# Kernel tuning notes

Measured on AMD Instinct MI355X. Metric: run time of the kernel, lower is better.

Reference implementation:

```python
import jax, jax.numpy as jnp
import numpy as np

D_MODEL = 1024
NUM_HEADS = 16
HEAD_DIM = D_MODEL // NUM_HEADS
B, S = 2, 2048
EPS = 1e-8


def setup_inputs() -> dict:
    key = jax.random.key(0)
    ks = jax.random.split(key, 9)
    sc = 1.0 / np.sqrt(D_MODEL)
    return {
        "x": jax.random.normal(ks[0], (B, S, D_MODEL), jnp.float32),
        "wq": jax.random.normal(ks[1], (D_MODEL, D_MODEL), jnp.float32) * sc,
        "bq": jax.random.normal(ks[2], (D_MODEL,), jnp.float32) * 0.01,
        "wk": jax.random.normal(ks[3], (D_MODEL, D_MODEL), jnp.float32) * sc,
        "bk": jax.random.normal(ks[4], (D_MODEL,), jnp.float32) * 0.01,
        "wv": jax.random.normal(ks[5], (D_MODEL, D_MODEL), jnp.float32) * sc,
        "bv": jax.random.normal(ks[6], (D_MODEL,), jnp.float32) * 0.01,
        "wo": jax.random.normal(ks[7], (D_MODEL, D_MODEL), jnp.float32) * sc,
        "bo": jax.random.normal(ks[8], (D_MODEL,), jnp.float32) * 0.01,
    }


def reference(x, wq, bq, wk, bk, wv, bv, wo, bo):
    b, s, d = x.shape
    h, hd = NUM_HEADS, HEAD_DIM
    # projections (torch Linear: y = x W^T + b); reshape to [b, h, s, hd]
    def proj(w, bias):
        return (jnp.einsum('bsd,ed->bse', x, w) + bias).reshape(b, s, h, hd).transpose(0, 2, 1, 3)
    q = proj(wq, bq)
    k = proj(wk, bk)
    v = proj(wv, bv)
    scores = jnp.einsum('bhqd,bhkd->bhqk', q, k) / np.sqrt(hd)
    attn = jax.nn.softmax(scores, axis=-1)
    o = jnp.einsum('bhqk,bhkd->bhqd', attn, v)  # [b, h, s, hd]
    # per-position, per-head Gram-Schmidt exclusion: remove component of o[i]
    # along v[i] (the loop in the original is independent over positions)
    v_norm_sq = jnp.sum(v * v, axis=-1, keepdims=True)          # [b,h,s,1]
    align = jnp.sum(o * v, axis=-1, keepdims=True) / (v_norm_sq + EPS)
    o = o - align * v
    o = o.transpose(0, 2, 1, 3).reshape(b, s, d)
    return jnp.einsum('bsd,ed->bse', o, wo) + bo
```

## Files before the change

kernel.cpp:

```cpp
#include <hip/hip_runtime.h>
#include <stdint.h>

#define SEQ 2048
#define NTOK 4096
#define DM 1024

typedef __bf16 bf16x8 __attribute__((ext_vector_type(8)));
typedef __bf16 bf16x4 __attribute__((ext_vector_type(4)));
typedef float f32x4 __attribute__((ext_vector_type(4)));

__device__ __forceinline__ unsigned short f2bf(float f) {
  union { float f; unsigned u; } v; v.f = f;
  return (unsigned short)((v.u + 0x7fffu + ((v.u >> 16) & 1u)) >> 16);
}
__device__ __forceinline__ float bf2f(unsigned short s) {
  union { unsigned u; float f; } v; v.u = ((unsigned)s) << 16; return v.f;
}
__device__ __forceinline__ unsigned pkbf(float a, float b) {
  union { float f; unsigned u; } x, y; x.f = a; y.f = b;
  return __builtin_amdgcn_perm(y.u + 0x8000u, x.u + 0x8000u, 0x07060302u);
}

__device__ __forceinline__ void async16(const unsigned short* g, unsigned short* l) {
  __builtin_amdgcn_global_load_lds(
      (const __attribute__((address_space(1))) void*)g,
      (__attribute__((address_space(3))) void*)l, 16, 0, 0);
}

__global__ __launch_bounds__(256) void cast_all(
    const float* __restrict__ x, const float* __restrict__ wq,
    const float* __restrict__ wk, const float* __restrict__ wv,
    const float* __restrict__ wo, unsigned short* __restrict__ dst) {
  size_t i = ((size_t)blockIdx.x * 256 + threadIdx.x) * 4;
  const float* src; size_t off;
  if (i < (size_t)NTOK * DM) { src = x; off = i; }
  else {
    size_t j = i - (size_t)NTOK * DM;
    int s = (int)(j >> 20);
    src = (s == 0) ? wq : (s == 1) ? wk : (s == 2) ? wv : wo;
    off = j & 1048575u;
  }
  float4 f = *(const float4*)(src + off);
  ushort4 o;
  o.x = f2bf(f.x); o.y = f2bf(f.y); o.z = f2bf(f.z); o.w = f2bf(f.w);
  *(ushort4*)(dst + i) = o;
}


template<int MI>
__device__ __forceinline__ void stage_half(
    const unsigned short* __restrict__ A, const unsigned short* __restrict__ Bw,
    int m0, int n0, int kt, unsigned short* As, unsigned short* Bs) {
  const int tid = threadIdx.x;
  const int r = tid >> 2, c = tid & 3;
#pragma unroll
  for (int b = 0; b < MI / 2; ++b) {
    const int row = b * 64 + r;
    async16(A + (size_t)(m0 + row) * 1024 + kt + ((c ^ (row & 3)) << 3),
            As + row * 32 + c * 8);
  }
#pragma unroll
  for (int b = 0; b < 2; ++b) {
    const int row = b * 64 + r;
    async16(Bw + (size_t)(n0 + row) * 1024 + kt + ((c ^ (row & 3)) << 3),
            Bs + row * 32 + c * 8);
  }
}

__device__ __forceinline__ void pipe_bar0() {
  asm volatile("s_waitcnt vmcnt(0)\ns_barrier" ::: "memory");
}
template<int MI>
__device__ __forceinline__ void pipe_barN() {
  if constexpr (MI == 4) asm volatile("s_waitcnt vmcnt(4)\ns_barrier" ::: "memory");
  else                   asm volatile("s_waitcnt vmcnt(3)\ns_barrier" ::: "memory");
}

template<int MI>
__device__ __forceinline__ void gemm_pipe(
    const unsigned short* __restrict__ A, const unsigned short* __restrict__ Bw,
    int m0, int n0, f32x4 (&acc)[MI][4],
    unsigned short* AsBase, unsigned short* BsBase) {
  const int tid = threadIdx.x, lane = tid & 63, w = tid >> 6;
  const int wm16 = (w >> 1) * MI * 16, wn = (w & 1) * 64;
  const int quad = lane >> 4, l16 = lane & 15;
  constexpr int ASZ = MI * 32 * 32;
  constexpr int BSZ = 128 * 32;

  stage_half<MI>(A, Bw, m0, n0, 0,  AsBase,       BsBase);
  stage_half<MI>(A, Bw, m0, n0, 32, AsBase + ASZ, BsBase + BSZ);
  pipe_barN<MI>();

  int cur = 0;
  for (int p = 0; p < 32; ++p) {
    const unsigned short* As = AsBase + cur * ASZ;
    const unsigned short* Bs = BsBase + cur * BSZ;

    bf16x8 af[MI], bf[4];
    const int swz = ((quad ^ (l16 & 3)) << 3);
#pragma unroll
    for (int i = 0; i < MI; ++i)
      af[i] = *(const bf16x8*)(As + (wm16 + i * 16 + l16) * 32 + swz);
#pragma unroll
    for (int j = 0; j < 4; ++j)
      bf[j] = *(const bf16x8*)(Bs + (wn + j * 16 + l16) * 32 + swz);

    if (p + 2 < 32) {
      const int slot = (cur == 0) ? 2 : cur - 1;
      stage_half<MI>(A, Bw, m0, n0, (p + 2) * 32,
                     AsBase + slot * ASZ, BsBase + slot * BSZ);
    }

#pragma unroll
    for (int i = 0; i < MI; ++i)
#pragma unroll
      for (int j = 0; j < 4; ++j)
        acc[i][j] = __builtin_amdgcn_mfma_f32_16x16x32_bf16(af[i], bf[j], acc[i][j], 0, 0, 0);

    if (p < 30)       pipe_barN<MI>();
    else if (p == 30) pipe_bar0();
    cur = (cur == 2) ? 0 : cur + 1;
  }
}

__device__ __forceinline__ void stage_half_qk(
    const unsigned short* __restrict__ A, const unsigned short* __restrict__ Bq,
    const unsigned short* __restrict__ Bk,
    int m0, int n0, int kt, unsigned short* As, unsigned short* Bqs,
    unsigned short* Bks) {
  const int tid = threadIdx.x;
  const int r = tid >> 2, c = tid & 3;
#pragma unroll
  for (int b = 0; b < 2; ++b) {
    const int row = b * 64 + r;
    const int off = kt + ((c ^ (row & 3)) << 3);
    async16(A + (size_t)(m0 + row) * 1024 + off, As + row * 32 + c * 8);
    async16(Bq + (size_t)(n0 + row) * 1024 + off, Bqs + row * 32 + c * 8);
    async16(Bk + (size_t)(n0 + row) * 1024 + off, Bks + row * 32 + c * 8);
  }
}
__device__ __forceinline__ void pipe_barQK() {
  asm volatile("s_waitcnt vmcnt(6)\ns_barrier" ::: "memory");
}

__device__ __forceinline__ void gemm_pipe_qk(
    const unsigned short* __restrict__ A, const unsigned short* __restrict__ Bq,
    const unsigned short* __restrict__ Bk,
    int m0, int n0, f32x4 (&accQ)[4][4], f32x4 (&accK)[4][4],
    unsigned short* AsBase, unsigned short* BqBase, unsigned short* BkBase) {
  const int tid = threadIdx.x, lane = tid & 63, w = tid >> 6;
  const int wm16 = (w >> 1) * 64, wn = (w & 1) * 64;
  const int quad = lane >> 4, l16 = lane & 15;
  constexpr int SZ = 128 * 32;

  stage_half_qk(A, Bq, Bk, m0, n0, 0,  AsBase,      BqBase,      BkBase);
  stage_half_qk(A, Bq, Bk, m0, n0, 32, AsBase + SZ, BqBase + SZ, BkBase + SZ);
  pipe_barQK();

  int cur = 0;
  for (int p = 0; p < 32; ++p) {
    const unsigned short* As = AsBase + cur * SZ;
    const unsigned short* Bqs = BqBase + cur * SZ;
    const unsigned short* Bks = BkBase + cur * SZ;

    bf16x8 af[4], bq[4], bk[4];
    const int swz = ((quad ^ (l16 & 3)) << 3);
#pragma unroll
    for (int i = 0; i < 4; ++i)
      af[i] = *(const bf16x8*)(As + (wm16 + i * 16 + l16) * 32 + swz);
#pragma unroll
    for (int j = 0; j < 4; ++j) {
      bq[j] = *(const bf16x8*)(Bqs + (wn + j * 16 + l16) * 32 + swz);
      bk[j] = *(const bf16x8*)(Bks + (wn + j * 16 + l16) * 32 + swz);
    }

    if (p + 2 < 32) {
      const int slot = (cur == 0) ? 2 : cur - 1;
      stage_half_qk(A, Bq, Bk, m0, n0, (p + 2) * 32,
                    AsBase + slot * SZ, BqBase + slot * SZ, BkBase + slot * SZ);
    }

#pragma unroll
    for (int i = 0; i < 4; ++i)
#pragma unroll
      for (int j = 0; j < 4; ++j) {
        accQ[i][j] = __builtin_amdgcn_mfma_f32_16x16x32_bf16(af[i], bq[j], accQ[i][j], 0, 0, 0);
        accK[i][j] = __builtin_amdgcn_mfma_f32_16x16x32_bf16(af[i], bk[j], accK[i][j], 0, 0, 0);
      }

    if (p < 30)       pipe_barQK();
    else if (p == 30) pipe_bar0();
    cur = (cur == 2) ? 0 : cur + 1;
  }
}

__global__ __launch_bounds__(256, 2) void qkv_gemm(
    const unsigned short* __restrict__ xb,
    const unsigned short* __restrict__ wqb, const unsigned short* __restrict__ wkb,
    const unsigned short* __restrict__ wvb,
    const float* __restrict__ bq, const float* __restrict__ bk, const float* __restrict__ bv,
    unsigned short* __restrict__ Q, unsigned short* __restrict__ Kd,
    unsigned short* __restrict__ Vt) {
  __shared__ unsigned short SH[9 * 128 * 32];
  const int gx = blockIdx.x;
  const int rr = gx & 255;
  const int tok = 4 * (rr & 7) + ((rr >> 3) & 3);
  const int oth = rr >> 5;
  const int lane = threadIdx.x & 63, w = threadIdx.x >> 6;
  const int quad = lane >> 4, l16 = lane & 15;
  const int wm = (w >> 1) * 64, wn = (w & 1) * 64;

  if (gx < 256) {
    const int m0 = tok * 128, n0 = oth * 128;
    f32x4 accQ[4][4], accK[4][4];
#pragma unroll
    for (int i = 0; i < 4; ++i)
#pragma unroll
      for (int j = 0; j < 4; ++j) {
        f32x4 z = {0.f, 0.f, 0.f, 0.f};
        accQ[i][j] = z; accK[i][j] = z;
      }
    gemm_pipe_qk(xb, wqb, wkb, m0, n0, accQ, accK,
                 SH, SH + 3 * 4096, SH + 6 * 4096);

#pragma unroll
    for (int i = 0; i < 4; ++i)
#pragma unroll
      for (int j = 0; j < 4; ++j) {
        const int col = n0 + wn + j * 16 + l16;
        const float bbq = bq[col], bbk = bk[col];
        const int h = col >> 6, d = col & 63;
#pragma unroll
        for (int r = 0; r < 4; ++r) {
          const int m = m0 + wm + i * 16 + quad * 4 + r;
          const int b = m >> 11, s = m & 2047;
          const int bh = b * 16 + h;
          Q[((size_t)bh * SEQ + s) * 64 + d] =
              f2bf((accQ[i][j][r] + bbq) * 0.180336880f);
          Kd[((size_t)bh * SEQ + s) * 64 + d] = f2bf(accK[i][j][r] + bbk);
        }
      }
  } else {
    const int m0 = oth * 128, n0 = tok * 128;
    f32x4 acc[4][4];
#pragma unroll
    for (int i = 0; i < 4; ++i)
#pragma unroll
      for (int j = 0; j < 4; ++j) { f32x4 z = {0.f, 0.f, 0.f, 0.f}; acc[i][j] = z; }
    gemm_pipe<4>(wvb, xb, m0, n0, acc, SH, SH + 3 * 4096);

#pragma unroll
    for (int i = 0; i < 4; ++i)
#pragma unroll
      for (int j = 0; j < 4; ++j) {
        const int n = n0 + wn + j * 16 + l16;
        const int tb = n >> 11, s = n & 2047;
#pragma unroll
        for (int r = 0; r < 4; ++r) {
          const int m = m0 + wm + i * 16 + quad * 4 + r;
          const int h = m >> 6, d = m & 63;
          Vt[((size_t)(tb * 16 + h) * 64 + d) * SEQ + s] = f2bf(acc[i][j][r] + bv[m]);
        }
      }
  }
}

__global__ __launch_bounds__(256, 2) void attn_kernel(
    const unsigned short* __restrict__ Q, const unsigned short* __restrict__ Kd,
    const unsigned short* __restrict__ Vt,
    unsigned short* __restrict__ O) {
  __shared__ unsigned short SH[32768];
#define KKB(g, b) (SH + ((g) * 2 + (b)) * 4096)
#define VVB(g, b) (SH + 16384 + ((g) * 2 + (b)) * 4096)
  const int gx = blockIdx.x;
  const int xcd = gx & 7;
  const int idx = gx >> 3;
  const int bh  = xcd * 4 + (idx & 3);
  const int q0  = (idx >> 2) * 128;
  const int tid = threadIdx.x, lane = tid & 63, w = tid >> 6;
  const int kp = w >> 1;
  const int wq = w & 1;
  const int quad = lane >> 4, l16 = lane & 15;
  const unsigned short* Qp = Q + (size_t)bh * SEQ * 64;
  const unsigned short* Kp = Kd + (size_t)bh * SEQ * 64;
  const unsigned short* Vp = Vt + (size_t)bh * 64 * SEQ;
  const int srow = tid >> 3;
  const int sc = ((tid & 7) ^ ((srow & 3) | ((srow & 8) >> 1))) << 3;

#pragma unroll
  for (int c = 0; c < 4; ++c)
    async16(Qp + (size_t)(q0 + c * 32 + srow) * 64 + sc,
            KKB(0, c >> 1) + (c & 1) * 2048 + tid * 8);
  __syncthreads();

  const int gl = (l16 & 3) | ((l16 & 8) >> 1);
  const int sel = l16 & 7;
  const unsigned short* Qsrc = KKB(0, wq);
  bf16x8 bQ[4][2];
#pragma unroll
  for (int qq = 0; qq < 4; ++qq) {
    const int qrow = qq * 16 + l16;
#pragma unroll
    for (int hh = 0; hh < 2; ++hh)
      bQ[qq][hh] = *(const bf16x8*)(Qsrc + qrow * 64 + (((hh * 4 + quad) ^ gl) << 3));
  }
  __syncthreads();

  auto stageKV = [&](int it_, int nb) {
#pragma unroll
    for (int g = 0; g < 2; ++g) {
      const int kt = g * 1024 + it_ * 64;
      async16(Kp + (size_t)(kt + srow) * 64 + sc, KKB(g, nb) + tid * 8);
      async16(Kp + (size_t)(kt + 32 + srow) * 64 + sc, KKB(g, nb) + 2048 + tid * 8);
      async16(Vp + (size_t)srow * SEQ + kt + sc, VVB(g, nb) + tid * 8);
      async16(Vp + (size_t)(32 + srow) * SEQ + kt + sc, VVB(g, nb) + 2048 + tid * 8);
    }
  };
  stageKV(0, 0);

  union { unsigned short u[8]; bf16x8 v; } one8;
#pragma unroll
  for (int t = 0; t < 8; ++t) one8.u[t] = 0x3F80;
  const bf16x8 aOnes = one8.v;

  f32x4 o_acc[4][4];
  f32x4 l_acc[4];
  const f32x4 zinit = {-12.f, -12.f, -12.f, -12.f};
#pragma unroll
  for (int qq = 0; qq < 4; ++qq) {
    f32x4 z = {0.f, 0.f, 0.f, 0.f};
    l_acc[qq] = z;
#pragma unroll
    for (int dt = 0; dt < 4; ++dt) o_acc[qq][dt] = z;
  }

  for (int it = 0; it < 16; ++it) {
    const int cur = it & 1;
    __syncthreads();
    if (it + 1 < 16) stageKV(it + 1, (it + 1) & 1);
    const unsigned short* Ks = KKB(kp, cur);
    const unsigned short* Vs = VVB(kp, cur);

    __builtin_amdgcn_s_setprio(1);

    bf16x8 bP[4][2];
#pragma unroll
    for (int ee = 0; ee < 4; ++ee) {
      const int G = ee >> 1, e = ee & 1;
      const int R = G * 32 + ((l16 >> 2) << 3) + e * 4 + (l16 & 3);
      const unsigned short* arow = Ks + R * 64;
      bf16x8 a0 = *(const bf16x8*)(arow + ((quad ^ sel) << 3));
      bf16x8 a1 = *(const bf16x8*)(arow + (((4 + quad) ^ sel) << 3));
#pragma unroll
      for (int qq = 0; qq < 4; ++qq) {
        f32x4 z = __builtin_amdgcn_mfma_f32_16x16x32_bf16(a0, bQ[qq][0], zinit, 0, 0, 0);
        z = __builtin_amdgcn_mfma_f32_16x16x32_bf16(a1, bQ[qq][1], z, 0, 0, 0);
        const unsigned u0 = (unsigned)(int)__builtin_fmaf(z[0], 8388608.0f, 1065024977.0f);
        const unsigned u1 = (unsigned)(int)__builtin_fmaf(z[1], 8388608.0f, 1065024977.0f);
        const unsigned u2 = (unsigned)(int)__builtin_fmaf(z[2], 8388608.0f, 1065024977.0f);
        const unsigned u3 = (unsigned)(int)__builtin_fmaf(z[3], 8388608.0f, 1065024977.0f);
        union { unsigned d[4]; bf16x8 v; } pk;
        pk.v = bP[qq][G];
        pk.d[e * 2]     = __builtin_amdgcn_perm(u1, u0, 0x07060302u);
        pk.d[e * 2 + 1] = __builtin_amdgcn_perm(u3, u2, 0x07060302u);
        bP[qq][G] = pk.v;
      }
    }

#pragma unroll
    for (int qq = 0; qq < 4; ++qq)
#pragma unroll
      for (int G = 0; G < 2; ++G)
        l_acc[qq] = __builtin_amdgcn_mfma_f32_16x16x32_bf16(aOnes, bP[qq][G], l_acc[qq], 0, 0, 0);

#pragma unroll
    for (int dt = 0; dt < 4; ++dt) {
      const unsigned short* vbase = Vs + (dt * 16 + l16) * 64;
#pragma unroll
      for (int G = 0; G < 2; ++G) {
        bf16x8 aV = *(const bf16x8*)(vbase + (((G * 4 + quad) ^ gl) << 3));
#pragma unroll
        for (int qq = 0; qq < 4; ++qq)
          o_acc[qq][dt] = __builtin_amdgcn_mfma_f32_16x16x32_bf16(aV, bP[qq][G], o_acc[qq][dt], 0, 0, 0);
      }
    }

    __builtin_amdgcn_s_setprio(0);
  }

  __syncthreads();
  float* xf = (float*)SH;
  if (kp == 1) {
    float* dst = xf + (size_t)(wq * 64 + lane) * 68;
#pragma unroll
    for (int qq = 0; qq < 4; ++qq)
#pragma unroll
      for (int dt = 0; dt < 4; ++dt)
        *(f32x4*)(dst + qq * 16 + dt * 4) = o_acc[qq][dt];
    f32x4 lv = {l_acc[0][0], l_acc[1][0], l_acc[2][0], l_acc[3][0]};
    *(f32x4*)(dst + 64) = lv;
  }
  __syncthreads();
  if (kp == 0) {
    const float* src = xf + (size_t)(wq * 64 + lane) * 68;
#pragma unroll
    for (int qq = 0; qq < 4; ++qq)
#pragma unroll
      for (int dt = 0; dt < 4; ++dt)
        o_acc[qq][dt] += *(const f32x4*)(src + qq * 16 + dt * 4);
    const f32x4 lv = *(const f32x4*)(src + 64);

    const int b = bh >> 4, h = bh & 15;
#pragma unroll
    for (int qq = 0; qq < 4; ++qq) {
      const int qg = q0 + wq * 64 + qq * 16 + l16;
      const float inv = 1.0f / (l_acc[qq][0] + lv[qq]);
      const unsigned short* vp = Vp + qg;
      float ov = 0.f, v2 = 0.f;
#pragma unroll
      for (int dt = 0; dt < 4; ++dt)
#pragma unroll
        for (int r = 0; r < 4; ++r) {
          const int d = dt * 16 + quad * 4 + r;
          const float v = bf2f(vp[(size_t)d * SEQ]);
          ov += o_acc[qq][dt][r] * v;
          v2 += v * v;
        }
      ov *= inv;
      ov += __shfl_xor(ov, 16); ov += __shfl_xor(ov, 32);
      v2 += __shfl_xor(v2, 16); v2 += __shfl_xor(v2, 32);
      const float align = ov / (v2 + 1e-8f);
      unsigned short* dst = O + (size_t)(b * SEQ + qg) * DM + h * 64;
#pragma unroll
      for (int dt = 0; dt < 4; ++dt) {
        float a[4];
#pragma unroll
        for (int r = 0; r < 4; ++r) {
          const int d = dt * 16 + quad * 4 + r;
          const float v = bf2f(vp[(size_t)d * SEQ]);
          a[r] = __builtin_fmaf(o_acc[qq][dt][r], inv, -align * v);
        }
        uint2 pk2;
        pk2.x = pkbf(a[0], a[1]);
        pk2.y = pkbf(a[2], a[3]);
        *(uint2*)(dst + dt * 16 + quad * 4) = pk2;
      }
    }
  }
#undef KKB
#undef VVB
}

__global__ __launch_bounds__(256) void out_gemm(
    const unsigned short* __restrict__ Ob, const unsigned short* __restrict__ wob,
    const float* __restrict__ bo, float* __restrict__ out) {
  __shared__ unsigned short As[3 * 64 * 32], Bs[3 * 128 * 32];
  const int m0 = blockIdx.y * 64, n0 = blockIdx.x * 128;
  f32x4 acc[2][4];
#pragma unroll
  for (int i = 0; i < 2; ++i)
#pragma unroll
    for (int j = 0; j < 4; ++j) { f32x4 z = {0.f, 0.f, 0.f, 0.f}; acc[i][j] = z; }

  gemm_pipe<2>(Ob, wob, m0, n0, acc, As, Bs);

  const int lane = threadIdx.x & 63, w = threadIdx.x >> 6;
  const int quad = lane >> 4, l16 = lane & 15;
  const int wm = (w >> 1) * 32, wn = (w & 1) * 64;
#pragma unroll
  for (int i = 0; i < 2; ++i)
#pragma unroll
    for (int j = 0; j < 4; ++j) {
      const int col = n0 + wn + j * 16 + l16;
      const float bb = bo[col];
#pragma unroll
      for (int r = 0; r < 4; ++r) {
        const int m = m0 + wm + i * 16 + quad * 4 + r;
        out[(size_t)m * DM + col] = acc[i][j][r] + bb;
      }
    }
}

extern "C" void kernel_launch(void* const* d_in, const int* in_sizes, int n_in,
                              void* d_out, int out_size, void* d_ws, size_t ws_size,
                              hipStream_t stream) {
  const float* x  = (const float*)d_in[0];
  const float* wq = (const float*)d_in[1];
  const float* bq = (const float*)d_in[2];
  const float* wk = (const float*)d_in[3];
  const float* bk = (const float*)d_in[4];
  const float* wv = (const float*)d_in[5];
  const float* bv = (const float*)d_in[6];
  const float* wo = (const float*)d_in[7];
  const float* bo = (const float*)d_in[8];
  float* out = (float*)d_out;
  (void)in_sizes; (void)n_in; (void)out_size; (void)ws_size;

  unsigned short* ws  = (unsigned short*)d_ws;
  unsigned short* xb  = ws;
  unsigned short* wqb = xb + (size_t)NTOK * DM;
  unsigned short* wkb = wqb + (size_t)DM * DM;
  unsigned short* wvb = wkb + (size_t)DM * DM;
  unsigned short* wob = wvb + (size_t)DM * DM;
  unsigned short* Qb  = wob + (size_t)DM * DM;
  unsigned short* Kb  = Qb + (size_t)NTOK * DM;
  unsigned short* Vtb = Kb + (size_t)NTOK * DM;
  unsigned short* Ob  = Vtb + (size_t)NTOK * DM;

  cast_all<<<8192, 256, 0, stream>>>(x, wq, wk, wv, wo, ws);
  qkv_gemm<<<512, 256, 0, stream>>>(xb, wqb, wkb, wvb, bq, bk, bv, Qb, Kb, Vtb);
  attn_kernel<<<512, 256, 0, stream>>>(Qb, Kb, Vtb, Ob);
  out_gemm<<<dim3(8, 64), 256, 0, stream>>>(Ob, wob, bo, out);
}
```

Before: 177.7 us.

## Software-pipeline attention loop: overlap PV MFMAs of previous tile with QK of current

Restructures the KV loop so the P·V and row-sum MFMAs for iteration it-1 run after the QK score computation of iteration it. V fragments and the packed P values are carried in registers across iterations, with an epilogue after the loop. The goal is to overlap the exp/pack ALU work with independent matrix instructions and hide LDS latency for V. The cost is more live registers (extra bf16x8 arrays plus an unroll of 2), which could lower occupancy or cause spills.

```diff
diff --git a/kernel.cpp b/kernel.cpp
--- a/kernel.cpp
+++ b/kernel.cpp
@@ -334,6 +334,10 @@
     for (int dt = 0; dt < 4; ++dt) o_acc[qq][dt] = z;
   }
 
+  bf16x8 bPo[4][2];
+  bf16x8 aVo[4][2];
+
+#pragma unroll 2
   for (int it = 0; it < 16; ++it) {
     const int cur = it & 1;
     __syncthreads();
@@ -343,7 +347,7 @@
 
     __builtin_amdgcn_s_setprio(1);
 
-    bf16x8 bP[4][2];
+    bf16x8 bPn[4][2];
 #pragma unroll
     for (int ee = 0; ee < 4; ++ee) {
       const int G = ee >> 1, e = ee & 1;
@@ -360,33 +364,58 @@
         const unsigned u2 = (unsigned)(int)__builtin_fmaf(z[2], 8388608.0f, 1065024977.0f);
         const unsigned u3 = (unsigned)(int)__builtin_fmaf(z[3], 8388608.0f, 1065024977.0f);
         union { unsigned d[4]; bf16x8 v; } pk;
-        pk.v = bP[qq][G];
+        pk.v = bPn[qq][G];
         pk.d[e * 2]     = __builtin_amdgcn_perm(u1, u0, 0x07060302u);
         pk.d[e * 2 + 1] = __builtin_amdgcn_perm(u3, u2, 0x07060302u);
-        bP[qq][G] = pk.v;
-      }
-    }
-
-#pragma unroll
-    for (int qq = 0; qq < 4; ++qq)
-#pragma unroll
-      for (int G = 0; G < 2; ++G)
-        l_acc[qq] = __builtin_amdgcn_mfma_f32_16x16x32_bf16(aOnes, bP[qq][G], l_acc[qq], 0, 0, 0);
+        bPn[qq][G] = pk.v;
+      }
+    }
+
+    if (it > 0) {
+#pragma unroll
+      for (int qq = 0; qq < 4; ++qq)
+#pragma unroll
+        for (int G = 0; G < 2; ++G)
+          l_acc[qq] = __builtin_amdgcn_mfma_f32_16x16x32_bf16(aOnes, bPo[qq][G], l_acc[qq], 0, 0, 0);
+#pragma unroll
+      for (int dt = 0; dt < 4; ++dt)
+#pragma unroll
+        for (int G = 0; G < 2; ++G)
+#pragma unroll
+          for (int qq = 0; qq < 4; ++qq)
+            o_acc[qq][dt] = __builtin_amdgcn_mfma_f32_16x16x32_bf16(aVo[dt][G], bPo[qq][G], o_acc[qq][dt], 0, 0, 0);
+    }
 
 #pragma unroll
     for (int dt = 0; dt < 4; ++dt) {
       const unsigned short* vbase = Vs + (dt * 16 + l16) * 64;
 #pragma unroll
-      for (int G = 0; G < 2; ++G) {
-        bf16x8 aV = *(const bf16x8*)(vbase + (((G * 4 + quad) ^ gl) << 3));
-#pragma unroll
-        for (int qq = 0; qq < 4; ++qq)
-          o_acc[qq][dt] = __builtin_amdgcn_mfma_f32_16x16x32_bf16(aV, bP[qq][G], o_acc[qq][dt], 0, 0, 0);
-      }
-    }
+      for (int G = 0; G < 2; ++G)
+        aVo[dt][G] = *(const bf16x8*)(vbase + (((G * 4 + quad) ^ gl) << 3));
+    }
+#pragma unroll
+    for (int qq = 0; qq < 4; ++qq)
+#pragma unroll
+      for (int G = 0; G < 2; ++G)
+        bPo[qq][G] = bPn[qq][G];
 
     __builtin_amdgcn_s_setprio(0);
   }
+
+  __builtin_amdgcn_s_setprio(1);
+#pragma unroll
+  for (int qq = 0; qq < 4; ++qq)
+#pragma unroll
+    for (int G = 0; G < 2; ++G)
+      l_acc[qq] = __builtin_amdgcn_mfma_f32_16x16x32_bf16(aOnes, bPo[qq][G], l_acc[qq], 0, 0, 0);
+#pragma unroll
+  for (int dt = 0; dt < 4; ++dt)
+#pragma unroll
+    for (int G = 0; G < 2; ++G)
+#pragma unroll
+      for (int qq = 0; qq < 4; ++qq)
+        o_acc[qq][dt] = __builtin_amdgcn_mfma_f32_16x16x32_bf16(aVo[dt][G], bPo[qq][G], o_acc[qq][dt], 0, 0, 0);
+  __builtin_amdgcn_s_setprio(0);
 
   __syncthreads();
   float* xf = (float*)SH;
```

New measurement: 204.8 us. 15.3% more time.
